# Performance work log

Hardware: AMD Instinct MI355X
Metric: run time of the kernel (lower is better)

## Reference

```python
import jax, jax.numpy as jnp
import numpy as np

G = 1024        # graphs in batch
NPG = 64        # nodes per graph
EPG = 256       # edges per graph
N = G * NPG     # 65536 total nodes
E = G * EPG     # 262144 total edges
IN_CH = 768
CH = 128
RATIO = 0.5
K = int(RATIO * EPG)  # edges reserved as 'causal' per graph


def setup_inputs() -> dict:
    key = jax.random.key(0)
    ks = jax.random.split(key, 10)
    w = lambda k, shape, fan: (jax.random.normal(k, shape, jnp.float32) / np.float32(np.sqrt(fan)))
    x = jax.random.normal(ks[0], (N, IN_CH), jnp.float32)
    # per-graph random edges, offset into the global node index space
    ei = jax.random.randint(ks[1], (2, G, EPG), 0, NPG)
    edge_index = (ei + (jnp.arange(G) * NPG)[None, :, None]).reshape(2, -1).astype(jnp.int32)
    edge_attr = jax.random.uniform(ks[2], (E,), jnp.float32)  # positive edge weights
    batch = jnp.repeat(jnp.arange(G, dtype=jnp.int32), NPG)
    return dict(
        x=x, edge_index=edge_index, edge_attr=edge_attr, batch=batch,
        W1=w(ks[3], (IN_CH, CH), IN_CH), V1=w(ks[4], (IN_CH, CH), IN_CH), b1=jnp.zeros((CH,), jnp.float32),
        W2=w(ks[5], (CH, CH), CH),       V2=w(ks[6], (CH, CH), CH),       b2=jnp.zeros((CH,), jnp.float32),
        mw1=w(ks[7], (2 * CH, 4 * CH), 2 * CH), mb1=jnp.zeros((4 * CH,), jnp.float32),
        mw2=w(ks[8], (4 * CH, 1), 4 * CH),      mb2=jnp.zeros((1,), jnp.float32),
    )


def reference(x, edge_index, edge_attr, batch, W1, V1, b1, W2, V2, b2, mw1, mb1, mw2, mb2):
    row, col = edge_index[0], edge_index[1]
    ew = edge_attr.reshape(-1)

    # gcn_norm (symmetric, no self loops), as used inside ARMAConv
    deg = jnp.zeros((N,), x.dtype).at[col].add(ew)
    dis = jnp.where(deg > 0, jax.lax.rsqrt(jnp.where(deg > 0, deg, 1.0)), 0.0)
    norm = dis[row] * ew * dis[col]  # [E]

    def arma(h, W, V, b):
        # ARMAConv, num_stacks=1, num_layers=1: ReLU(A_hat (h W) + h V + b)
        m = h @ W                                            # [N, C]
        agg = jnp.zeros((N, W.shape[1]), h.dtype).at[col].add(norm[:, None] * m[row])
        return jax.nn.relu(agg + h @ V + b)

    x1 = jax.nn.relu(arma(x, W1, V1, b1))  # outer F.relu (idempotent after internal ReLU)
    x2 = arma(x1, W2, V2, b2)              # [N, CH]

    # edge-gather MLP -> scalar score per edge
    edge_rep = jnp.concatenate([x2[row], x2[col]], axis=-1)          # [E, 2C]
    pred_edge_weight = (jax.nn.relu(edge_rep @ mw1 + mb1) @ mw2 + mb2).reshape(-1)  # [E]

    # per-graph top-k split (batched replacement of the numpy argpartition loop)
    wg = pred_edge_weight.reshape(G, EPG)
    order = jnp.argsort(-wg, axis=1)                                  # descending
    base = (jnp.arange(G) * EPG)[:, None]
    cid = (base + order[:, :K]).reshape(-1)   # causal (reserved) edge ids
    did = (base + order[:, K:]).reshape(-1)   # conf (dropped) edge ids

    causal = (x2, edge_index[:, cid], edge_attr[cid], pred_edge_weight[cid], batch)
    conf = (x2, edge_index[:, did], edge_attr[did], -pred_edge_weight[did], batch)
    return (*causal, *conf, pred_edge_weight)
```

## Files before the change

kernel.cpp:

```cpp
#include <hip/hip_runtime.h>
#include <hip/hip_bf16.h>
#include <stdint.h>

#define G_    1024
#define NPG   64
#define EPG   256
#define N_    (G_*NPG)
#define E_    (G_*EPG)
#define IN_CH 768
#define CH    128
#define KSEL  128
#define HID   512

#define NCH  (N_*CH)
#define GK   (G_*KSEL)
#define OFF0 0
#define OFF1 (OFF0 + NCH)
#define OFF2 (OFF1 + 2*GK)
#define OFF3 (OFF2 + GK)
#define OFF4 (OFF3 + GK)
#define OFF5 (OFF4 + N_)
#define OFF6 (OFF5 + NCH)
#define OFF7 (OFF6 + 2*GK)
#define OFF8 (OFF7 + GK)
#define OFF9 (OFF8 + GK)
#define OFF10 (OFF9 + N_)

typedef unsigned short u16;
typedef unsigned int   u32;
typedef __attribute__((ext_vector_type(8))) short bf16x8;
typedef __attribute__((ext_vector_type(4))) float f32x4;

__device__ __forceinline__ u16 f2bf(float x) {
    union { float f; u32 u; } v; v.f = x;
    u32 r = v.u + 0x7fffu + ((v.u >> 16) & 1u);
    return (u16)(r >> 16);
}
__device__ __forceinline__ float bf2f(u32 h) {
    union { u32 u; float f; } v; v.u = h << 16; return v.f;
}
__device__ __forceinline__ u16 bfc(float x) {
    __hip_bfloat16 h = __float2bfloat16(x);
    return *reinterpret_cast<u16*>(&h);
}

__global__ void k_deg(const int* __restrict__ ei, const float* __restrict__ ea,
                      float* __restrict__ deg) {
    int e = blockIdx.x * 256 + threadIdx.x;
    if (e < E_) atomicAdd(&deg[ei[E_ + e]], ea[e]);
}

__global__ void k_dis(float* __restrict__ deg) {
    int i = blockIdx.x * 256 + threadIdx.x;
    if (i < N_) { float d = deg[i]; deg[i] = d > 0.f ? 1.0f / sqrtf(d) : 0.f; }
}

__global__ void k_norm(const int* __restrict__ ei, const float* __restrict__ ea,
                       const float* __restrict__ dis, float* __restrict__ norm) {
    int e = blockIdx.x * 256 + threadIdx.x;
    if (e < E_) norm[e] = dis[ei[e]] * ea[e] * dis[ei[E_ + e]];
}

__global__ void k_concat(const float* __restrict__ W1, const float* __restrict__ V1,
                         const float* __restrict__ W2, const float* __restrict__ V2,
                         const float* __restrict__ mw1,
                         u16* __restrict__ WV1t, u16* __restrict__ WV2t,
                         u16* __restrict__ Mwt) {
    int i = blockIdx.x * 256 + threadIdx.x;
    if (i < 256 * IN_CH) {
        int c = i / IN_CH, r = i - c * IN_CH;
        WV1t[i] = f2bf(c < CH ? W1[r*CH + c] : V1[r*CH + (c - CH)]);
    }
    if (i < 256 * CH) {
        int c = i >> 7, r = i & 127;
        WV2t[i] = f2bf(c < CH ? W2[r*CH + c] : V2[r*CH + (c - CH)]);
    }
    if (i < 1024 * CH) {
        int c = i >> 7, r = i & 127;
        Mwt[i] = f2bf(c < HID ? mw1[r*HID + c] : mw1[(CH + r)*HID + (c - HID)]);
    }
}

__global__ __launch_bounds__(256) void k_gemm1(const float* __restrict__ Ap,
        const u16* __restrict__ Bt, u16* __restrict__ Cp) {
    __shared__ float As[3][128 * 32];
    const int t = threadIdx.x;
    const int lane = t & 63, w = t >> 6;
    const int wr = (w >> 1) << 6, wc = (w & 1) << 6;
    const size_t bm = (size_t)blockIdx.x * 128;
    const size_t bn = (size_t)blockIdx.y * 128;
    const int r16 = lane & 15, kq = lane >> 4;

    int cid[4], grow[4], gcol[4];
    #pragma unroll
    for (int i = 0; i < 4; ++i) {
        int c = i * 256 + t;
        cid[i] = c;
        int row = c >> 3, sl = c & 7;
        grow[i] = row;
        gcol[i] = (sl ^ (row & 7)) * 4;
    }

    f32x4 acc[4][4];
    #pragma unroll
    for (int m = 0; m < 4; ++m)
        #pragma unroll
        for (int n = 0; n < 4; ++n)
            acc[m][n] = (f32x4){0.f, 0.f, 0.f, 0.f};

    #define STAGE(buf, k0)                                                      \
        do {                                                                    \
            _Pragma("unroll")                                                   \
            for (int i = 0; i < 4; ++i) {                                       \
                const float* src = Ap + (bm + grow[i]) * (size_t)IN_CH + (k0) + gcol[i]; \
                __builtin_amdgcn_global_load_lds(                               \
                    (const __attribute__((address_space(1))) void*)src,         \
                    (__attribute__((address_space(3))) void*)&As[buf][cid[i] * 4], \
                    16, 0, 0);                                                  \
            }                                                                   \
        } while (0)

    #define LOADB(bv, k0)                                                       \
        do {                                                                    \
            _Pragma("unroll")                                                   \
            for (int n = 0; n < 4; ++n)                                         \
                bv[n] = *(const bf16x8*)(Bt + (bn + wc + n * 16 + r16) * (size_t)IN_CH + (k0) + kq * 8); \
        } while (0)

    STAGE(0, 0);
    bf16x8 bc[4];
    LOADB(bc, 0);
    STAGE(1, 32);
    asm volatile("s_waitcnt vmcnt(4)" ::: "memory");
    __builtin_amdgcn_sched_barrier(0);
    __builtin_amdgcn_s_barrier();

    const int nk = IN_CH / 32;
    int srd = 0, sst = 2;
    #pragma unroll 1
    for (int ki = 0; ki < nk; ++ki) {
        bf16x8 bnx[4];
        if (ki + 1 < nk) LOADB(bnx, (ki + 1) * 32);
        if (ki + 2 < nk) STAGE(sst, (ki + 2) * 32);

        bf16x8 a[4];
        #pragma unroll
        for (int m = 0; m < 4; ++m) {
            int row = wr + m * 16 + r16;
            int xr = row & 7;
            const float* base = &As[srd][row * 32];
            float4 q0 = *(const float4*)(base + (((2 * kq)     ^ xr) * 4));
            float4 q1 = *(const float4*)(base + (((2 * kq + 1) ^ xr) * 4));
            union { bf16x8 v; u16 s[8]; } pk;
            pk.s[0] = bfc(q0.x); pk.s[1] = bfc(q0.y); pk.s[2] = bfc(q0.z); pk.s[3] = bfc(q0.w);
            pk.s[4] = bfc(q1.x); pk.s[5] = bfc(q1.y); pk.s[6] = bfc(q1.z); pk.s[7] = bfc(q1.w);
            a[m] = pk.v;
        }
        #pragma unroll
        for (int m = 0; m < 4; ++m)
            #pragma unroll
            for (int n = 0; n < 4; ++n)
                acc[m][n] = __builtin_amdgcn_mfma_f32_16x16x32_bf16(a[m], bc[n], acc[m][n], 0, 0, 0);
        if (ki + 1 < nk) {
            #pragma unroll
            for (int n = 0; n < 4; ++n) bc[n] = bnx[n];
        }
        if (ki + 2 < nk) { asm volatile("s_waitcnt vmcnt(4)" ::: "memory"); }
        else             { asm volatile("s_waitcnt vmcnt(0)" ::: "memory"); }
        __builtin_amdgcn_sched_barrier(0);
        __builtin_amdgcn_s_barrier();
        __builtin_amdgcn_sched_barrier(0);
        srd = (srd == 2) ? 0 : srd + 1;
        sst = (sst == 2) ? 0 : sst + 1;
    }
    #undef STAGE
    #undef LOADB

    #pragma unroll
    for (int m = 0; m < 4; ++m)
        #pragma unroll
        for (int j = 0; j < 4; ++j) {
            size_t row = bm + wr + m * 16 + kq * 4 + j;
            #pragma unroll
            for (int n = 0; n < 4; ++n) {
                size_t col = bn + wc + n * 16 + r16;
                Cp[row * 256 + col] = f2bf(acc[m][n][j]);
            }
        }
}

__global__ __launch_bounds__(256) void k_agg1(const int* __restrict__ ei,
        const float* __restrict__ norm, const u16* __restrict__ Bb,
        const float* __restrict__ bias, u16* __restrict__ x1b) {
    __shared__ float A_s[64 * 65];
    __shared__ u16   Ms[64 * 132];
    const int g = blockIdx.x, t = threadIdx.x;
    const int lane = t & 63, w = t >> 6;
    const int r16 = lane & 15, kq = lane >> 4;
    const size_t nbase = (size_t)g * 64;

    for (int i = t; i < 64 * 65; i += 256) A_s[i] = 0.f;
    for (int i = t; i < 64 * 32; i += 256) {
        int row = i >> 5, c4 = (i & 31) << 2;
        *(uint2*)&Ms[row * 132 + c4] = *(const uint2*)(Bb + (nbase + row) * 256 + c4);
    }
    __syncthreads();
    { int e = g * 256 + t;
      atomicAdd(&A_s[(ei[e] & 63) * 65 + (ei[E_ + e] & 63)], norm[e]); }
    __syncthreads();

    const int n0 = w * 32;
    f32x4 acc[4][2];
    #pragma unroll
    for (int mt = 0; mt < 4; ++mt)
        #pragma unroll
        for (int nt = 0; nt < 2; ++nt)
            acc[mt][nt] = (f32x4){0.f, 0.f, 0.f, 0.f};

    union bfr { bf16x8 v; u16 s[8]; };
    #pragma unroll
    for (int ks = 0; ks < 2; ++ks) {
        bfr a[4], b[2];
        #pragma unroll
        for (int mt = 0; mt < 4; ++mt)
            #pragma unroll
            for (int i = 0; i < 8; ++i)
                a[mt].s[i] = f2bf(A_s[(ks*32 + kq*8 + i) * 65 + mt*16 + r16]);
        #pragma unroll
        for (int nt = 0; nt < 2; ++nt)
            #pragma unroll
            for (int i = 0; i < 8; ++i)
                b[nt].s[i] = Ms[(ks*32 + kq*8 + i) * 132 + n0 + nt*16 + r16];
        #pragma unroll
        for (int mt = 0; mt < 4; ++mt)
            #pragma unroll
            for (int nt = 0; nt < 2; ++nt)
                acc[mt][nt] = __builtin_amdgcn_mfma_f32_16x16x32_bf16(a[mt].v, b[nt].v, acc[mt][nt], 0, 0, 0);
    }
    #pragma unroll
    for (int mt = 0; mt < 4; ++mt)
        #pragma unroll
        for (int j = 0; j < 4; ++j) {
            int c = mt * 16 + kq * 4 + j;
            size_t node = nbase + c;
            #pragma unroll
            for (int nt = 0; nt < 2; ++nt) {
                int ch = n0 + nt * 16 + r16;
                float v = bf2f(Bb[node * 256 + 128 + ch]) + bias[ch];
                x1b[node * 128 + ch] = f2bf(fmaxf(acc[mt][nt][j] + v, 0.f));
            }
        }
}

__global__ __launch_bounds__(256) void k_l2agg(const u16* __restrict__ x1b,
        const u16* __restrict__ Wt, const int* __restrict__ ei,
        const float* __restrict__ norm, const float* __restrict__ bias,
        float* __restrict__ out0, float* __restrict__ out5,
        u16* __restrict__ xb) {
    __shared__ float A_s[64 * 65];
    __shared__ u16   MVs[64 * 264];
    const int g = blockIdx.x, t = threadIdx.x;
    const int lane = t & 63, w = t >> 6;
    const int r16 = lane & 15, kq = lane >> 4;
    const size_t nbase = (size_t)g * 64;

    for (int i = t; i < 64 * 65; i += 256) A_s[i] = 0.f;
    __syncthreads();
    { int e = g * 256 + t;
      atomicAdd(&A_s[(ei[e] & 63) * 65 + (ei[E_ + e] & 63)], norm[e]); }

    const int wc = w * 64;
    f32x4 acc[4][4];
    #pragma unroll
    for (int mt = 0; mt < 4; ++mt)
        #pragma unroll
        for (int n = 0; n < 4; ++n)
            acc[mt][n] = (f32x4){0.f, 0.f, 0.f, 0.f};
    #pragma unroll
    for (int ks = 0; ks < 4; ++ks) {
        int k0 = ks * 32;
        bf16x8 a[4], b[4];
        #pragma unroll
        for (int mt = 0; mt < 4; ++mt)
            a[mt] = *(const bf16x8*)(x1b + (nbase + mt * 16 + r16) * 128 + k0 + kq * 8);
        #pragma unroll
        for (int n = 0; n < 4; ++n)
            b[n] = *(const bf16x8*)(Wt + (size_t)(wc + n * 16 + r16) * 128 + k0 + kq * 8);
        #pragma unroll
        for (int mt = 0; mt < 4; ++mt)
            #pragma unroll
            for (int n = 0; n < 4; ++n)
                acc[mt][n] = __builtin_amdgcn_mfma_f32_16x16x32_bf16(a[mt], b[n], acc[mt][n], 0, 0, 0);
    }
    #pragma unroll
    for (int mt = 0; mt < 4; ++mt)
        #pragma unroll
        for (int j = 0; j < 4; ++j) {
            int row = mt * 16 + kq * 4 + j;
            #pragma unroll
            for (int n = 0; n < 4; ++n)
                MVs[row * 264 + wc + n * 16 + r16] = f2bf(acc[mt][n][j]);
        }
    __syncthreads();

    const int n0 = w * 32;
    f32x4 ag[4][2];
    #pragma unroll
    for (int mt = 0; mt < 4; ++mt)
        #pragma unroll
        for (int nt = 0; nt < 2; ++nt)
            ag[mt][nt] = (f32x4){0.f, 0.f, 0.f, 0.f};
    union bfr { bf16x8 v; u16 s[8]; };
    #pragma unroll
    for (int ks = 0; ks < 2; ++ks) {
        bfr a[4], b[2];
        #pragma unroll
        for (int mt = 0; mt < 4; ++mt)
            #pragma unroll
            for (int i = 0; i < 8; ++i)
                a[mt].s[i] = f2bf(A_s[(ks*32 + kq*8 + i) * 65 + mt*16 + r16]);
        #pragma unroll
        for (int nt = 0; nt < 2; ++nt)
            #pragma unroll
            for (int i = 0; i < 8; ++i)
                b[nt].s[i] = MVs[(ks*32 + kq*8 + i) * 264 + n0 + nt*16 + r16];
        #pragma unroll
        for (int mt = 0; mt < 4; ++mt)
            #pragma unroll
            for (int nt = 0; nt < 2; ++nt)
                ag[mt][nt] = __builtin_amdgcn_mfma_f32_16x16x32_bf16(a[mt].v, b[nt].v, ag[mt][nt], 0, 0, 0);
    }
    #pragma unroll
    for (int mt = 0; mt < 4; ++mt)
        #pragma unroll
        for (int j = 0; j < 4; ++j) {
            int c = mt * 16 + kq * 4 + j;
            size_t node = nbase + c;
            #pragma unroll
            for (int nt = 0; nt < 2; ++nt) {
                int ch = n0 + nt * 16 + r16;
                float v = bf2f(MVs[c * 264 + 128 + ch]) + bias[ch];
                float r = fmaxf(ag[mt][nt][j] + v, 0.f);
                out0[node * 128 + ch] = r;
                out5[node * 128 + ch] = r;
                xb[node * 128 + ch] = f2bf(r);
            }
        }
}

#define PQS 1032
__global__ __launch_bounds__(512) void k_pqedge(const u16* __restrict__ x2b,
        const u16* __restrict__ Mwt, const int* __restrict__ ei,
        const float* __restrict__ mb1, const float* __restrict__ mw2,
        const float* __restrict__ mb2, float* __restrict__ pred) {
    __shared__ u16 PQs[64 * PQS];
    __shared__ float mw2s[512];
    const int g = blockIdx.x, t = threadIdx.x;
    const int lane = t & 63, w = t >> 6;
    const int r16 = lane & 15, kq = lane >> 4;
    const int nb = w * 128;

    if (t < 128) *(float4*)&mw2s[t * 4] = *(const float4*)&mw2[t * 4];

    f32x4 acc[4][8];
    #pragma unroll
    for (int mt = 0; mt < 4; ++mt)
        #pragma unroll
        for (int nt = 0; nt < 8; ++nt)
            acc[mt][nt] = (f32x4){0.f, 0.f, 0.f, 0.f};

    #pragma unroll
    for (int ks = 0; ks < 4; ++ks) {
        const int k0 = ks * 32;
        bf16x8 a[4], b[8];
        #pragma unroll
        for (int mt = 0; mt < 4; ++mt)
            a[mt] = *(const bf16x8*)(x2b + ((size_t)g * 64 + mt * 16 + r16) * 128 + k0 + kq * 8);
        #pragma unroll
        for (int nt = 0; nt < 8; ++nt)
            b[nt] = *(const bf16x8*)(Mwt + (size_t)(nb + nt * 16 + r16) * 128 + k0 + kq * 8);
        #pragma unroll
        for (int mt = 0; mt < 4; ++mt)
            #pragma unroll
            for (int nt = 0; nt < 8; ++nt)
                acc[mt][nt] = __builtin_amdgcn_mfma_f32_16x16x32_bf16(a[mt], b[nt], acc[mt][nt], 0, 0, 0);
    }
    #pragma unroll
    for (int nt = 0; nt < 8; ++nt) {
        int col = nb + nt * 16 + r16;
        float bias = (col < HID) ? mb1[col] : 0.f;
        #pragma unroll
        for (int mt = 0; mt < 4; ++mt)
            #pragma unroll
            for (int j = 0; j < 4; ++j) {
                int row = mt * 16 + kq * 4 + j;
                PQs[row * PQS + col] = f2bf(acc[mt][nt][j] + bias);
            }
    }
    __syncthreads();

    const int le = lane & 31, jh = lane >> 5;
    const int e = g * 256 + w * 32 + le;
    const int r = ei[e] & 63, c = ei[E_ + e] & 63;
    const u16* pP = &PQs[r * PQS + jh * 256];
    const u16* pQ = &PQs[c * PQS + 512 + jh * 256];
    const float* pW = &mw2s[jh * 256];
    float s = 0.f;
    #pragma unroll 8
    for (int it = 0; it < 32; ++it) {
        uint4 up = *(const uint4*)(pP + it * 8);
        uint4 uq = *(const uint4*)(pQ + it * 8);
        float4 w0 = *(const float4*)(pW + it * 8);
        float4 w1 = *(const float4*)(pW + it * 8 + 4);
        u32 pu[4] = {up.x, up.y, up.z, up.w};
        u32 qu[4] = {uq.x, uq.y, uq.z, uq.w};
        float ww[8] = {w0.x,w0.y,w0.z,w0.w,w1.x,w1.y,w1.z,w1.w};
        #pragma unroll
        for (int k = 0; k < 4; ++k) {
            float p0 = bf2f(pu[k] & 0xffffu), p1 = bf2f(pu[k] >> 16);
            float q0 = bf2f(qu[k] & 0xffffu), q1 = bf2f(qu[k] >> 16);
            s += fmaxf(p0 + q0, 0.f) * ww[2*k];
            s += fmaxf(p1 + q1, 0.f) * ww[2*k + 1];
        }
    }
    s += __shfl_xor(s, 32, 64);
    if (lane < 32) pred[e] = s + mb2[0];
}

__global__ __launch_bounds__(256) void k_sort(const float* __restrict__ pred,
        const int* __restrict__ ei, const float* __restrict__ ea,
        float* __restrict__ out) {
    __shared__ float key[256];
    __shared__ int   idx[256];
    int g = blockIdx.x, t = threadIdx.x;
    int ebase = g * EPG;
    float p = pred[ebase + t];
    key[t] = p; idx[t] = t;
    for (int k2 = 2; k2 <= 256; k2 <<= 1) {
        for (int j = k2 >> 1; j >= 1; j >>= 1) {
            __syncthreads();
            int ixj = t ^ j;
            if (ixj > t) {
                float ka = key[t], kb = key[ixj];
                int   ia = idx[t], ib = idx[ixj];
                bool up = ((t & k2) == 0);
                bool a_before_b = (ka > kb) || (ka == kb && ia < ib);
                bool do_swap = up ? !a_before_b : a_before_b;
                if (do_swap) { key[t] = kb; key[ixj] = ka; idx[t] = ib; idx[ixj] = ia; }
            }
        }
    }
    __syncthreads();
    int el = idx[t];
    int eg = ebase + el;
    float pv = key[t];
    float r = (float)ei[eg];
    float c = (float)ei[E_ + eg];
    float av = ea[eg];
    if (t < KSEL) {
        int oo = g * KSEL + t;
        out[OFF1 + oo]      = r;
        out[OFF1 + GK + oo] = c;
        out[OFF2 + oo]      = av;
        out[OFF3 + oo]      = pv;
    } else {
        int oo = g * KSEL + (t - KSEL);
        out[OFF6 + oo]      = r;
        out[OFF6 + GK + oo] = c;
        out[OFF7 + oo]      = av;
        out[OFF8 + oo]      = -pv;
    }
    out[OFF10 + ebase + t] = p;
}

__global__ void k_batch(const int* __restrict__ batch, float* __restrict__ out) {
    int i = blockIdx.x * 256 + threadIdx.x;
    if (i < N_) { float b = (float)batch[i]; out[OFF4 + i] = b; out[OFF9 + i] = b; }
}

extern "C" void kernel_launch(void* const* d_in, const int* in_sizes, int n_in,
                              void* d_out, int out_size, void* d_ws, size_t ws_size,
                              hipStream_t stream) {
    const float* x     = (const float*)d_in[0];
    const int*   ei    = (const int*)  d_in[1];
    const float* ea    = (const float*)d_in[2];
    const int*   batch = (const int*)  d_in[3];
    const float* W1    = (const float*)d_in[4];
    const float* V1    = (const float*)d_in[5];
    const float* b1    = (const float*)d_in[6];
    const float* W2    = (const float*)d_in[7];
    const float* V2    = (const float*)d_in[8];
    const float* b2    = (const float*)d_in[9];
    const float* mw1   = (const float*)d_in[10];
    const float* mb1   = (const float*)d_in[11];
    const float* mw2   = (const float*)d_in[12];
    const float* mb2   = (const float*)d_in[13];
    float* out = (float*)d_out;

    char* ws = (char*)d_ws;
    size_t o = 0;
    float* deg  = (float*)(ws + o); o += (size_t)N_ * 4;
    float* norm = (float*)(ws + o); o += (size_t)E_ * 4;
    float* pred = (float*)(ws + o); o += (size_t)E_ * 4;
    u16* WV1t   = (u16*)(ws + o);   o += (size_t)256 * IN_CH * 2;
    u16* WV2t   = (u16*)(ws + o);   o += (size_t)256 * CH * 2;
    u16* Mwt    = (u16*)(ws + o);   o += (size_t)1024 * CH * 2;
    u16* x2b    = (u16*)(ws + o);   o += (size_t)N_ * CH * 2;
    u16* x1b    = (u16*)(ws + o);   o += (size_t)N_ * CH * 2;
    u16* B1b    = (u16*)(ws + o);   o += (size_t)N_ * 256 * 2;

    hipMemsetAsync(deg, 0, (size_t)N_ * 4, stream);
    k_deg <<<E_/256, 256, 0, stream>>>(ei, ea, deg);
    k_dis <<<N_/256, 256, 0, stream>>>(deg);
    k_norm<<<E_/256, 256, 0, stream>>>(ei, ea, deg, norm);
    k_concat<<<768, 256, 0, stream>>>(W1, V1, W2, V2, mw1, WV1t, WV2t, Mwt);

    dim3 g1(N_/128, 2);
    k_gemm1<<<g1, 256, 0, stream>>>(x, WV1t, B1b);
    k_agg1<<<G_, 256, 0, stream>>>(ei, norm, B1b, b1, x1b);
    k_l2agg<<<G_, 256, 0, stream>>>(x1b, WV2t, ei, norm, b2, out + OFF0, out + OFF5, x2b);
    k_pqedge<<<G_, 512, 0, stream>>>(x2b, Mwt, ei, mb1, mw2, mb2, pred);
    k_sort<<<G_, 256, 0, stream>>>(pred, ei, ea, out);
    k_batch<<<N_/256, 256, 0, stream>>>(batch, out);
}
```

Measured before the change: 257.0 us.

## Pre-convert input features to bf16 before first GEMM

```diff
diff --git a/kernel.cpp b/kernel.cpp
--- a/kernel.cpp
+++ b/kernel.cpp
@@ -39,10 +39,6 @@
 __device__ __forceinline__ float bf2f(u32 h) {
     union { u32 u; float f; } v; v.u = h << 16; return v.f;
 }
-__device__ __forceinline__ u16 bfc(float x) {
-    __hip_bfloat16 h = __float2bfloat16(x);
-    return *reinterpret_cast<u16*>(&h);
-}
 
 __global__ void k_deg(const int* __restrict__ ei, const float* __restrict__ ea,
                       float* __restrict__ deg) {
@@ -59,6 +55,22 @@
                        const float* __restrict__ dis, float* __restrict__ norm) {
     int e = blockIdx.x * 256 + threadIdx.x;
     if (e < E_) norm[e] = dis[ei[e]] * ea[e] * dis[ei[E_ + e]];
+}
+
+__global__ __launch_bounds__(256) void k_cvt(const float* __restrict__ x,
+                                             u16* __restrict__ xb) {
+    const size_t total = (size_t)N_ * IN_CH / 8;
+    size_t i = (size_t)blockIdx.x * 256 + threadIdx.x;
+    const size_t stride = (size_t)gridDim.x * 256;
+    for (; i < total; i += stride) {
+        const float* p = x + i * 8;
+        float4 a = *(const float4*)p;
+        float4 b = *(const float4*)(p + 4);
+        union { uint4 q; u16 s[8]; } pk;
+        pk.s[0]=f2bf(a.x); pk.s[1]=f2bf(a.y); pk.s[2]=f2bf(a.z); pk.s[3]=f2bf(a.w);
+        pk.s[4]=f2bf(b.x); pk.s[5]=f2bf(b.y); pk.s[6]=f2bf(b.z); pk.s[7]=f2bf(b.w);
+        *(uint4*)(xb + i * 8) = pk.q;
+    }
 }
 
 __global__ void k_concat(const float* __restrict__ W1, const float* __restrict__ V1,
@@ -81,9 +93,9 @@
     }
 }
 
-__global__ __launch_bounds__(256) void k_gemm1(const float* __restrict__ Ap,
+__global__ __launch_bounds__(256) void k_gemm1(const u16* __restrict__ Ap,
         const u16* __restrict__ Bt, u16* __restrict__ Cp) {
-    __shared__ float As[3][128 * 32];
+    __shared__ u16 As[3][128 * 32];
     const int t = threadIdx.x;
     const int lane = t & 63, w = t >> 6;
     const int wr = (w >> 1) << 6, wc = (w & 1) << 6;
@@ -91,14 +103,14 @@
     const size_t bn = (size_t)blockIdx.y * 128;
     const int r16 = lane & 15, kq = lane >> 4;
 
-    int cid[4], grow[4], gcol[4];
-    #pragma unroll
-    for (int i = 0; i < 4; ++i) {
+    int cid[2], grow[2], gcol[2];
+    #pragma unroll
+    for (int i = 0; i < 2; ++i) {
         int c = i * 256 + t;
         cid[i] = c;
-        int row = c >> 3, sl = c & 7;
+        int row = c >> 2, sl = c & 3;
         grow[i] = row;
-        gcol[i] = (sl ^ (row & 7)) * 4;
+        gcol[i] = (sl ^ (row & 3)) * 8;
     }
 
     f32x4 acc[4][4];
@@ -111,11 +123,11 @@
     #define STAGE(buf, k0)                                                      \
         do {                                                                    \
             _Pragma("unroll")                                                   \
-            for (int i = 0; i < 4; ++i) {                                       \
-                const float* src = Ap + (bm + grow[i]) * (size_t)IN_CH + (k0) + gcol[i]; \
+            for (int i = 0; i < 2; ++i) {                                       \
+                const u16* src = Ap + (bm + grow[i]) * (size_t)IN_CH + (k0) + gcol[i]; \
                 __builtin_amdgcn_global_load_lds(                               \
                     (const __attribute__((address_space(1))) void*)src,         \
-                    (__attribute__((address_space(3))) void*)&As[buf][cid[i] * 4], \
+                    (__attribute__((address_space(3))) void*)&As[buf][cid[i] * 8], \
                     16, 0, 0);                                                  \
             }                                                                   \
         } while (0)
@@ -131,7 +143,7 @@
     bf16x8 bc[4];
     LOADB(bc, 0);
     STAGE(1, 32);
-    asm volatile("s_waitcnt vmcnt(4)" ::: "memory");
+    asm volatile("s_waitcnt vmcnt(2)" ::: "memory");
     __builtin_amdgcn_sched_barrier(0);
     __builtin_amdgcn_s_barrier();
 
@@ -147,14 +159,7 @@
         #pragma unroll
         for (int m = 0; m < 4; ++m) {
             int row = wr + m * 16 + r16;
-            int xr = row & 7;
-            const float* base = &As[srd][row * 32];
-            float4 q0 = *(const float4*)(base + (((2 * kq)     ^ xr) * 4));
-            float4 q1 = *(const float4*)(base + (((2 * kq + 1) ^ xr) * 4));
-            union { bf16x8 v; u16 s[8]; } pk;
-            pk.s[0] = bfc(q0.x); pk.s[1] = bfc(q0.y); pk.s[2] = bfc(q0.z); pk.s[3] = bfc(q0.w);
-            pk.s[4] = bfc(q1.x); pk.s[5] = bfc(q1.y); pk.s[6] = bfc(q1.z); pk.s[7] = bfc(q1.w);
-            a[m] = pk.v;
+            a[m] = *(const bf16x8*)&As[srd][row * 32 + ((kq ^ (row & 3)) * 8)];
         }
         #pragma unroll
         for (int m = 0; m < 4; ++m)
@@ -165,7 +170,7 @@
             #pragma unroll
             for (int n = 0; n < 4; ++n) bc[n] = bnx[n];
         }
-        if (ki + 2 < nk) { asm volatile("s_waitcnt vmcnt(4)" ::: "memory"); }
+        if (ki + 2 < nk) { asm volatile("s_waitcnt vmcnt(2)" ::: "memory"); }
         else             { asm volatile("s_waitcnt vmcnt(0)" ::: "memory"); }
         __builtin_amdgcn_sched_barrier(0);
         __builtin_amdgcn_s_barrier();
@@ -505,18 +510,22 @@
     u16* WV1t   = (u16*)(ws + o);   o += (size_t)256 * IN_CH * 2;
     u16* WV2t   = (u16*)(ws + o);   o += (size_t)256 * CH * 2;
     u16* Mwt    = (u16*)(ws + o);   o += (size_t)1024 * CH * 2;
-    u16* x2b    = (u16*)(ws + o);   o += (size_t)N_ * CH * 2;
-    u16* x1b    = (u16*)(ws + o);   o += (size_t)N_ * CH * 2;
     u16* B1b    = (u16*)(ws + o);   o += (size_t)N_ * 256 * 2;
+    char* xreg  = ws + o;
+    u16* xb     = (u16*)xreg;
+    u16* x1b    = (u16*)xreg;
+    u16* x2b    = (u16*)(xreg + (size_t)N_ * CH * 2);
+    o += (size_t)N_ * IN_CH * 2;
 
     hipMemsetAsync(deg, 0, (size_t)N_ * 4, stream);
     k_deg <<<E_/256, 256, 0, stream>>>(ei, ea, deg);
     k_dis <<<N_/256, 256, 0, stream>>>(deg);
     k_norm<<<E_/256, 256, 0, stream>>>(ei, ea, deg, norm);
     k_concat<<<768, 256, 0, stream>>>(W1, V1, W2, V2, mw1, WV1t, WV2t, Mwt);
+    k_cvt<<<2048, 256, 0, stream>>>(x, xb);
 
     dim3 g1(N_/128, 2);
-    k_gemm1<<<g1, 256, 0, stream>>>(x, WV1t, B1b);
+    k_gemm1<<<g1, 256, 0, stream>>>(xb, WV1t, B1b);
     k_agg1<<<G_, 256, 0, stream>>>(ei, norm, B1b, b1, x1b);
     k_l2agg<<<G_, 256, 0, stream>>>(x1b, WV2t, ei, norm, b2, out + OFF0, out + OFF5, x2b);
     k_pqedge<<<G_, 512, 0, stream>>>(x2b, Mwt, ei, mb1, mw2, mb2, pred);
```

Result: slower. 291.6 us (+13.4%).
